# Optimization experiments

Hardware: AMD Instinct MI355X
Metric: run time of the kernel (lower is better)

## Reference

```python
import jax, jax.numpy as jnp
import numpy as np

# Analytic form of the 4-qubit circuit:
#   state |0000>; RZ(x_i) on wire i adds only a per-qubit global phase on |0>,
#   After RY(theta_i), <Z_i> = cos(theta_i) (product state). Conjugating Z_i
#   through CNOT(0,1),CNOT(1,2),CNOT(2,3),CNOT(3,0) (Heisenberg picture,
#   Z_t -> Z_c Z_t) gives with c_i = cos(theta_i):
#     <Z0> = c1*c2*c3,  <Z1> = c0*c1,  <Z2> = c0*c1*c2,  <Z3> = c0*c1*c2*c3
#   This matches PennyLane's default.qubit output exactly.

def _circuit_expvals(params):
    c = jnp.cos(params)  # (4,)
    return jnp.stack([c[1] * c[2] * c[3],
                      c[0] * c[1],
                      c[0] * c[1] * c[2],
                      c[0] * c[1] * c[2] * c[3]])  # (4,)


def setup_inputs() -> dict:
    key = jax.random.key(0)
    k_x, k_w1, k_w2, k_wo, k_p = jax.random.split(key, 5)
    B, S, E, F = 8, 2048, 1024, 4096
    x = jax.random.normal(k_x, (B, S, E), dtype=jnp.float32)
    # torch nn.Linear convention: weight shape (out_features, in_features)
    w1 = jax.random.normal(k_w1, (4, E), dtype=jnp.float32) * (1.0 / np.sqrt(E))
    w2 = jax.random.normal(k_w2, (F, 4), dtype=jnp.float32) * 0.5
    w_out = jax.random.normal(k_wo, (E, F), dtype=jnp.float32) * (1.0 / np.sqrt(F))
    params = jax.random.normal(k_p, (4,), dtype=jnp.float32)
    return {"x": x, "w1": w1, "w2": w2, "w_out": w_out, "params": params}


def reference(x, w1, w2, w_out, params):
    B, S, E = x.shape
    # linear1 is computed in the original but its output only enters the RZ
    # layer acting on |0>, which is a pure phase -> no effect on expvals.
    x_q = jnp.einsum('bse,fe->bsf', x, w1)  # (B,S,4), faithful dead path
    q = _circuit_expvals(params)            # (4,), same for every sample
    q_out = jnp.broadcast_to(q, x_q.shape)  # (B,S,4)
    h = jax.nn.relu(jnp.einsum('bsf,gf->bsg', q_out, w2))  # (B,S,ffn_dim)
    # dropout omitted (eval mode / p treated as 0 for deterministic reference)
    return jnp.einsum('bsg,eg->bse', h, w_out)  # (B,S,E)
```

## Files before the change

kernel.cpp:

```cpp
#include <hip/hip_runtime.h>
#include <hip/hip_bf16.h>

typedef float f32x4 __attribute__((ext_vector_type(4)));

#define E_DIM 1024
#define F_DIM 4096

__global__ __launch_bounds__(256) void qff_head(
    const float* __restrict__ w2,
    const float* __restrict__ wout,
    const float* __restrict__ params,
    float* __restrict__ o)
{
    __shared__ float h[F_DIM];

    const float c0 = cosf(params[0]);
    const float c1 = cosf(params[1]);
    const float c2 = cosf(params[2]);
    const float c3 = cosf(params[3]);
    const float q0 = c1 * c2 * c3;
    const float q1 = c0 * c1;
    const float q2 = q1 * c2;
    const float q3 = q2 * c3;

    const int t = threadIdx.x;
    const f32x4* w2v = reinterpret_cast<const f32x4*>(w2);
    for (int g = t; g < F_DIM; g += 256) {
        f32x4 w = w2v[g];
        float v = w.x * q0 + w.y * q1 + w.z * q2 + w.w * q3;
        h[g] = v > 0.0f ? v : 0.0f;
    }
    __syncthreads();

    const int wave = t >> 6;
    const int lane = t & 63;
    const int e = blockIdx.x * 4 + wave;
    const f32x4* h4 = reinterpret_cast<const f32x4*>(h);
    const f32x4* wrow = reinterpret_cast<const f32x4*>(wout + (size_t)e * F_DIM);

    float s = 0.0f;
#pragma unroll
    for (int j = 0; j < F_DIM / 4 / 64; ++j) {
        f32x4 a = wrow[lane + j * 64];
        f32x4 b = h4[lane + j * 64];
        s += a.x * b.x + a.y * b.y + a.z * b.z + a.w * b.w;
    }
#pragma unroll
    for (int off = 32; off > 0; off >>= 1) s += __shfl_down(s, off);
    if (lane == 0) o[e] = s;
}

__global__ __launch_bounds__(256) void qff_bcast(
    const float* __restrict__ o, float* __restrict__ out, int n4)
{
    const f32x4* o4 = reinterpret_cast<const f32x4*>(o);
    f32x4* out4 = reinterpret_cast<f32x4*>(out);
    const int stride = gridDim.x * 256;
    const int idx = blockIdx.x * 256 + threadIdx.x;
    const f32x4 v = o4[idx & (E_DIM / 4 - 1)];
    for (int i = idx; i < n4; i += stride) {
        __builtin_nontemporal_store(v, &out4[i]);
    }
}

extern "C" void kernel_launch(void* const* d_in, const int* in_sizes, int n_in,
                              void* d_out, int out_size, void* d_ws, size_t ws_size,
                              hipStream_t stream) {
    const float* w2     = (const float*)d_in[2];
    const float* w_out  = (const float*)d_in[3];
    const float* params = (const float*)d_in[4];
    float* o   = (float*)d_ws;
    float* out = (float*)d_out;

    qff_head<<<E_DIM / 4, 256, 0, stream>>>(w2, w_out, params, o);

    const int n4 = out_size / 4;
    qff_bcast<<<2048, 256, 0, stream>>>(o, out, n4);
}
```

Baseline: 26.23 us.

## Split each output row across four waves and compute h on the fly

The head kernel now launches one block per output element instead of one per four elements. The four waves each handle a quarter of the F dimension and combine partial sums through shared memory. Each block recomputes the needed h values directly from w2 rather than first building the full h vector in LDS behind a barrier. The w_out row is read with nontemporal loads. This gives more blocks and removes the serial h-build phase, at the cost of reading w2 redundantly (from cache) in every block. The broadcast kernel, which writes the large output, is unchanged and likely dominates the total time.

```diff
diff --git a/kernel.cpp b/kernel.cpp
--- a/kernel.cpp
+++ b/kernel.cpp
@@ -12,7 +12,11 @@
     const float* __restrict__ params,
     float* __restrict__ o)
 {
-    __shared__ float h[F_DIM];
+    __shared__ float psum[4];
+    const int t = threadIdx.x;
+    const int wave = t >> 6;
+    const int lane = t & 63;
+    const int e = blockIdx.x;
 
     const float c0 = cosf(params[0]);
     const float c1 = cosf(params[1]);
@@ -23,31 +27,29 @@
     const float q2 = q1 * c2;
     const float q3 = q2 * c3;
 
-    const int t = threadIdx.x;
-    const f32x4* w2v = reinterpret_cast<const f32x4*>(w2);
-    for (int g = t; g < F_DIM; g += 256) {
-        f32x4 w = w2v[g];
-        float v = w.x * q0 + w.y * q1 + w.z * q2 + w.w * q3;
-        h[g] = v > 0.0f ? v : 0.0f;
-    }
-    __syncthreads();
-
-    const int wave = t >> 6;
-    const int lane = t & 63;
-    const int e = blockIdx.x * 4 + wave;
-    const f32x4* h4 = reinterpret_cast<const f32x4*>(h);
     const f32x4* wrow = reinterpret_cast<const f32x4*>(wout + (size_t)e * F_DIM);
+    const f32x4* w2v  = reinterpret_cast<const f32x4*>(w2);
 
     float s = 0.0f;
 #pragma unroll
-    for (int j = 0; j < F_DIM / 4 / 64; ++j) {
-        f32x4 a = wrow[lane + j * 64];
-        f32x4 b = h4[lane + j * 64];
-        s += a.x * b.x + a.y * b.y + a.z * b.z + a.w * b.w;
+    for (int j = 0; j < 4; ++j) {
+        const int g4 = wave * 256 + j * 64 + lane;
+        f32x4 a  = __builtin_nontemporal_load(&wrow[g4]);
+        f32x4 r0 = w2v[4 * g4 + 0];
+        f32x4 r1 = w2v[4 * g4 + 1];
+        f32x4 r2 = w2v[4 * g4 + 2];
+        f32x4 r3 = w2v[4 * g4 + 3];
+        float h0 = fmaxf(r0.x * q0 + r0.y * q1 + r0.z * q2 + r0.w * q3, 0.0f);
+        float h1 = fmaxf(r1.x * q0 + r1.y * q1 + r1.z * q2 + r1.w * q3, 0.0f);
+        float h2 = fmaxf(r2.x * q0 + r2.y * q1 + r2.z * q2 + r2.w * q3, 0.0f);
+        float h3 = fmaxf(r3.x * q0 + r3.y * q1 + r3.z * q2 + r3.w * q3, 0.0f);
+        s += a.x * h0 + a.y * h1 + a.z * h2 + a.w * h3;
     }
 #pragma unroll
     for (int off = 32; off > 0; off >>= 1) s += __shfl_down(s, off);
-    if (lane == 0) o[e] = s;
+    if (lane == 0) psum[wave] = s;
+    __syncthreads();
+    if (t == 0) o[e] = psum[0] + psum[1] + psum[2] + psum[3];
 }
 
 __global__ __launch_bounds__(256) void qff_bcast(
@@ -72,7 +74,7 @@
     float* o   = (float*)d_ws;
     float* out = (float*)d_out;
 
-    qff_head<<<E_DIM / 4, 256, 0, stream>>>(w2, w_out, params, o);
+    qff_head<<<E_DIM, 256, 0, stream>>>(w2, w_out, params, o);
 
     const int n4 = out_size / 4;
     qff_bcast<<<2048, 256, 0, stream>>>(o, out, n4);
```

After: 27.39 us. 1.04x slower.

## Fuse head matvec and broadcast into a single tiled kernel

Applied to the files above, without the earlier changes.

Merges the matvec kernel and the broadcast-store kernel into one launch. Each block recomputes h, computes 16 output columns from w_out, and writes those columns for 1024 rows. This removes the second launch and the workspace round-trip. In exchange each w_out row is read by 16 blocks, h is recomputed in every block, and each store row covers only 64 contiguous bytes, which can hurt write coalescing.

```diff
diff --git a/kernel.cpp b/kernel.cpp
--- a/kernel.cpp
+++ b/kernel.cpp
@@ -5,14 +5,24 @@
 
 #define E_DIM 1024
 #define F_DIM 4096
+#define ROWS  16384
+#define NCG   64
+#define NRG   16
 
-__global__ __launch_bounds__(256) void qff_head(
+__global__ __launch_bounds__(256) void qff_fused(
     const float* __restrict__ w2,
     const float* __restrict__ wout,
     const float* __restrict__ params,
-    float* __restrict__ o)
+    float* __restrict__ out)
 {
     __shared__ float h[F_DIM];
+    __shared__ float o_l[16];
+
+    const int t = threadIdx.x;
+    const int wave = t >> 6;
+    const int lane = t & 63;
+    const int cg = blockIdx.x & (NCG - 1);
+    const int rg = blockIdx.x >> 6;
 
     const float c0 = cosf(params[0]);
     const float c1 = cosf(params[1]);
@@ -23,7 +33,6 @@
     const float q2 = q1 * c2;
     const float q3 = q2 * c3;
 
-    const int t = threadIdx.x;
     const f32x4* w2v = reinterpret_cast<const f32x4*>(w2);
     for (int g = t; g < F_DIM; g += 256) {
         f32x4 w = w2v[g];
@@ -32,34 +41,31 @@
     }
     __syncthreads();
 
-    const int wave = t >> 6;
-    const int lane = t & 63;
-    const int e = blockIdx.x * 4 + wave;
+    const int e0 = cg * 16;
     const f32x4* h4 = reinterpret_cast<const f32x4*>(h);
-    const f32x4* wrow = reinterpret_cast<const f32x4*>(wout + (size_t)e * F_DIM);
+    for (int i = wave; i < 16; i += 4) {
+        const f32x4* wrow = reinterpret_cast<const f32x4*>(wout + (size_t)(e0 + i) * F_DIM);
+        float s = 0.0f;
+#pragma unroll
+        for (int j = 0; j < F_DIM / 4 / 64; ++j) {
+            f32x4 a = wrow[lane + j * 64];
+            f32x4 b = h4[lane + j * 64];
+            s += a.x * b.x + a.y * b.y + a.z * b.z + a.w * b.w;
+        }
+#pragma unroll
+        for (int off = 32; off > 0; off >>= 1) s += __shfl_down(s, off);
+        if (lane == 0) o_l[i] = s;
+    }
+    __syncthreads();
 
-    float s = 0.0f;
+    const f32x4 v = reinterpret_cast<const f32x4*>(o_l)[t & 3];
+    const int q4 = cg * 4 + (t & 3);
+    const int r0 = rg * 1024 + (t >> 2);
+    f32x4* out4 = reinterpret_cast<f32x4*>(out);
 #pragma unroll
-    for (int j = 0; j < F_DIM / 4 / 64; ++j) {
-        f32x4 a = wrow[lane + j * 64];
-        f32x4 b = h4[lane + j * 64];
-        s += a.x * b.x + a.y * b.y + a.z * b.z + a.w * b.w;
-    }
-#pragma unroll
-    for (int off = 32; off > 0; off >>= 1) s += __shfl_down(s, off);
-    if (lane == 0) o[e] = s;
-}
-
-__global__ __launch_bounds__(256) void qff_bcast(
-    const float* __restrict__ o, float* __restrict__ out, int n4)
-{
-    const f32x4* o4 = reinterpret_cast<const f32x4*>(o);
-    f32x4* out4 = reinterpret_cast<f32x4*>(out);
-    const int stride = gridDim.x * 256;
-    const int idx = blockIdx.x * 256 + threadIdx.x;
-    const f32x4 v = o4[idx & (E_DIM / 4 - 1)];
-    for (int i = idx; i < n4; i += stride) {
-        __builtin_nontemporal_store(v, &out4[i]);
+    for (int k = 0; k < 16; ++k) {
+        const int r = r0 + k * 64;
+        __builtin_nontemporal_store(v, &out4[(size_t)r * (E_DIM / 4) + q4]);
     }
 }
 
@@ -69,11 +75,7 @@
     const float* w2     = (const float*)d_in[2];
     const float* w_out  = (const float*)d_in[3];
     const float* params = (const float*)d_in[4];
-    float* o   = (float*)d_ws;
     float* out = (float*)d_out;
 
-    qff_head<<<E_DIM / 4, 256, 0, stream>>>(w2, w_out, params, o);
-
-    const int n4 = out_size / 4;
-    qff_bcast<<<2048, 256, 0, stream>>>(o, out, n4);
+    qff_fused<<<NCG * NRG, 256, 0, stream>>>(w2, w_out, params, out);
 }
```

New measurement: 32.29 us. +23.1%, slower.
